# Kernel tuning notes

Hardware: AMD Instinct MI355X
Metric: run time of the kernel (lower is better)

Reference implementation:

```python
import jax, jax.numpy as jnp
import numpy as np

B, T, C = 64, 384, 256
NH, NKV = 4, 2
HD = C // NH            # 64
NREP = NH // NKV        # 2
NE, TOPK = 8, 2
HID = int(8 / 3 * C)    # 682
EPS_RMS = 1e-6


def _rope_tables(t_len):
    inv_freq = 1.0 / (10000.0 ** (np.arange(0, HD, 2, dtype=np.float32) / HD))
    t = np.arange(t_len, dtype=np.float32)
    freqs = np.outer(t, inv_freq)                      # [T, HD/2]
    emb = np.concatenate([freqs, freqs], axis=-1)      # [T, HD]
    return jnp.asarray(np.cos(emb)), jnp.asarray(np.sin(emb))


def _rotate_half(x):
    h = x.shape[-1] // 2
    return jnp.concatenate([-x[..., h:], x[..., :h]], axis=-1)


def _rmsnorm(v, w):
    return v * jax.lax.rsqrt(jnp.mean(v * v, axis=-1, keepdims=True) + EPS_RMS) * w


def setup_inputs() -> dict:
    key = jax.random.key(0)
    ks = jax.random.split(key, 10)
    s = lambda k, shape: (jax.random.normal(k, shape, jnp.float32) * 0.02)
    return {
        "x": jax.random.normal(ks[0], (B, T, C), jnp.float32),
        "ln1_w": jnp.ones((C,), jnp.float32),
        "ln2_w": jnp.ones((C,), jnp.float32),
        "wq": s(ks[1], (NH * HD, C)),
        "wk": s(ks[2], (NKV * HD, C)),
        "wv": s(ks[3], (NKV * HD, C)),
        "wo": s(ks[4], (C, C)),
        "router_w": s(ks[5], (NE, C)),
        "w1": s(ks[6], (NE, HID, C)),
        "w2": s(ks[7], (NE, C, HID)),
        "w3": s(ks[8], (NE, HID, C)),
    }


def reference(x, ln1_w, ln2_w, wq, wk, wv, wo, router_w, w1, w2, w3):
    Bx, Tx, Cx = x.shape
    # --- attention sub-block ---
    h = _rmsnorm(x, ln1_w)
    q = (h @ wq.T).reshape(Bx, Tx, NH, HD).transpose(0, 2, 1, 3)    # [B,H,T,D]
    k = (h @ wk.T).reshape(Bx, Tx, NKV, HD).transpose(0, 2, 1, 3)   # [B,KV,T,D]
    v = (h @ wv.T).reshape(Bx, Tx, NKV, HD).transpose(0, 2, 1, 3)
    cos, sin = _rope_tables(Tx)
    cos, sin = cos[None, None], sin[None, None]
    q = q * cos + _rotate_half(q) * sin
    k = k * cos + _rotate_half(k) * sin
    k = jnp.repeat(k, NREP, axis=1)   # GQA: expand kv heads
    v = jnp.repeat(v, NREP, axis=1)
    scores = jnp.einsum('bhtd,bhsd->bhts', q, k) / jnp.sqrt(jnp.float32(HD))
    causal = jnp.tril(jnp.ones((Tx, Tx), dtype=bool))
    scores = jnp.where(causal[None, None], scores, jnp.float32(-1e30))
    att = jax.nn.softmax(scores, axis=-1)
    y = jnp.einsum('bhts,bhsd->bhtd', att, v).transpose(0, 2, 1, 3).reshape(Bx, Tx, Cx)
    x = x + y @ wo.T

    # --- MoE sub-block ---
    flat = _rmsnorm(x, ln2_w).reshape(-1, Cx)                  # [N, C]
    probs = jax.nn.softmax(flat @ router_w.T, axis=-1)         # [N, NE]
    tp, ti = jax.lax.top_k(probs, TOPK)
    tp = tp / (jnp.sum(tp, axis=-1, keepdims=True) + 1e-9)
    # per-token per-expert combine weight (0 if not selected)
    weights = jnp.sum(tp[..., None] * jax.nn.one_hot(ti, NE, dtype=flat.dtype), axis=1)  # [N, NE]
    out = jnp.zeros_like(flat)
    for e in range(NE):  # small fixed expert count
        hh = jax.nn.silu(flat @ w1[e].T) * (flat @ w3[e].T)
        out = out + weights[:, e:e + 1] * (hh @ w2[e].T)
    return x + out.reshape(Bx, Tx, Cx)
```

## Files before the change

kernel.cpp:

```cpp
#include <hip/hip_runtime.h>
#include <hip/hip_bf16.h>
#include <math.h>

typedef unsigned short u16t;
typedef __bf16 bf16x8 __attribute__((ext_vector_type(8)));
typedef float f32x4 __attribute__((ext_vector_type(4)));

#define NBATCH 64
#define NT 384
#define NC 256
#define NHID 682
#define NHIDP 704
#define NTOK (NBATCH * NT)
#define NSLOT (2 * NTOK + 1024)

#define SB0 196
#define SB1 (SB0 + 512)
#define SB2 (SB1 + 256)
#define SB3 (SB2 + 5632)
#define SB4 (SB3 + 5632)
#define SB5 (SB4 + 48)
#define SB6 (SB5 + NTOK / 4)

static __device__ __forceinline__ float bf2f(u16t u) { return __uint_as_float(((unsigned int)u) << 16); }
static __device__ __forceinline__ u16t f2bf(float f) { return __builtin_bit_cast(u16t, __float2bfloat16(f)); }

static __device__ __forceinline__ void gload16(const void* gp, void* lp) {
  __builtin_amdgcn_global_load_lds((const __attribute__((address_space(1))) void*)gp,
                                   (__attribute__((address_space(3))) void*)lp, 16, 0, 0);
}

static __device__ __forceinline__ void pipe_barrier_full() {
  asm volatile("s_waitcnt vmcnt(0) lgkmcnt(0)" ::: "memory");
  __builtin_amdgcn_s_barrier();
  asm volatile("" ::: "memory");
}


__global__ __launch_bounds__(256) void k_setup(const float* __restrict__ wq, const float* __restrict__ wk,
                                               const float* __restrict__ wv, const float* __restrict__ wo,
                                               const float* __restrict__ w1, const float* __restrict__ w2,
                                               const float* __restrict__ w3,
                                               const float* __restrict__ x, const float* __restrict__ ln1w,
                                               int* __restrict__ tok, float* __restrict__ tokw,
                                               int* __restrict__ ctrl,
                                               u16t* __restrict__ wqkvb, u16t* __restrict__ wob,
                                               u16t* __restrict__ w1p, u16t* __restrict__ w3p,
                                               u16t* __restrict__ w2p, float* __restrict__ rtab,
                                               u16t* __restrict__ h) {
  int blk = blockIdx.x, t = threadIdx.x;
  if (blk < SB0) {
    int i = blk * 256 + t;
    tok[i] = -1; tokw[i] = 0.f;
    if (blk == 0 && t < 64) ctrl[t] = 0;
  } else if (blk < SB1) {
    int i = (blk - SB0) * 256 + t;
    int row = i >> 8, col = i & 255;
    float s = (row < 256) ? wq[(size_t)row * 256 + col]
            : (row < 384) ? wk[(size_t)(row - 256) * 256 + col]
                          : wv[(size_t)(row - 384) * 256 + col];
    wqkvb[i] = f2bf(s);
  } else if (blk < SB2) {
    int i = (blk - SB1) * 256 + t;
    wob[i] = f2bf(wo[i]);
  } else if (blk < SB3) {
    int idx = (blk - SB2) * 256 + t;
    int kcol = idx & 255; int tmp = idx >> 8; int nrow = tmp % NHIDP; int e = tmp / NHIDP;
    if (nrow < NHID) {
      size_t src = ((size_t)e * NHID + nrow) * NC + kcol;
      w1p[idx] = f2bf(w1[src]); w3p[idx] = f2bf(w3[src]);
    } else { w1p[idx] = 0; w3p[idx] = 0; }
  } else if (blk < SB4) {
    int idx = (blk - SB3) * 256 + t;
    int kcol = idx % NHIDP; int tmp = idx / NHIDP; int nrow = tmp & 255; int e = tmp >> 8;
    w2p[idx] = (kcol < NHID) ? f2bf(w2[((size_t)e * NC + nrow) * NHID + kcol]) : (u16t)0;
  } else if (blk < SB5) {
    int i = (blk - SB4) * 256 + t;
    int tt = i >> 5, d = i & 31;
    float ang = (float)tt * powf(10000.f, -(float)d * (1.f / 32.f));
    float s, c; sincosf(ang, &s, &c);
    ((float2*)rtab)[i] = make_float2(c, s);
  } else {
    int w = t >> 6, l = t & 63;
    int n = (blk - SB5) * 4 + w;
    const float* xr = x + (size_t)n * NC;
    float4 xa = *(const float4*)(xr + l * 4);
    float ssq = xa.x * xa.x + xa.y * xa.y + xa.z * xa.z + xa.w * xa.w;
    for (int d = 1; d < 64; d <<= 1) ssq += __shfl_xor(ssq, d, 64);
    float rs = rsqrtf(ssq * (1.f / 256.f) + 1e-6f);
    float4 wa = *(const float4*)(ln1w + l * 4);
    ushort4 o;
    o.x = f2bf(xa.x * rs * wa.x);
    o.y = f2bf(xa.y * rs * wa.y);
    o.z = f2bf(xa.z * rs * wa.z);
    o.w = f2bf(xa.w * rs * wa.w);
    *(ushort4*)(h + (size_t)n * NC + l * 4) = o;
  }
}

__global__ __launch_bounds__(256) void k_rms_router(const float* __restrict__ xin,
                                                    const float* __restrict__ wg,
                                                    const float* __restrict__ rw,
                                                    u16t* __restrict__ flat,
                                                    int* __restrict__ eidx,
                                                    float* __restrict__ ew) {
  int w = threadIdx.x >> 6, l = threadIdx.x & 63;
  int n = blockIdx.x * 4 + w;
  const float* xr = xin + (size_t)n * NC;
  float4 xa = *(const float4*)(xr + l * 4);
  float ssq = xa.x * xa.x + xa.y * xa.y + xa.z * xa.z + xa.w * xa.w;
  for (int d = 1; d < 64; d <<= 1) ssq += __shfl_xor(ssq, d, 64);
  float rs = rsqrtf(ssq * (1.f / 256.f) + 1e-6f);
  float4 wa = *(const float4*)(wg + l * 4);
  float n0 = xa.x * rs * wa.x, n1 = xa.y * rs * wa.y;
  float n2 = xa.z * rs * wa.z, n3 = xa.w * rs * wa.w;
  ushort4 o; o.x = f2bf(n0); o.y = f2bf(n1); o.z = f2bf(n2); o.w = f2bf(n3);
  *(ushort4*)(flat + (size_t)n * NC + l * 4) = o;
  float acc[8];
  for (int e = 0; e < 8; e++) {
    float4 ra = *(const float4*)(rw + (size_t)e * NC + l * 4);
    acc[e] = n0 * ra.x + n1 * ra.y + n2 * ra.z + n3 * ra.w;
  }
  for (int e = 0; e < 8; e++)
    for (int d = 1; d < 64; d <<= 1) acc[e] += __shfl_xor(acc[e], d, 64);
  if (l == 0) {
    float mx = acc[0];
    for (int e = 1; e < 8; e++) mx = fmaxf(mx, acc[e]);
    float p[8], sum = 0.f;
    for (int e = 0; e < 8; e++) { p[e] = __expf(acc[e] - mx); sum += p[e]; }
    float inv = 1.f / sum;
    for (int e = 0; e < 8; e++) p[e] *= inv;
    int i0 = 0; float b0 = p[0];
    for (int e = 1; e < 8; e++) if (p[e] > b0) { b0 = p[e]; i0 = e; }
    int i1 = -1; float b1 = -1.f;
    for (int e = 0; e < 8; e++) if (e != i0 && p[e] > b1) { b1 = p[e]; i1 = e; }
    float s2 = 1.f / (b0 + b1 + 1e-9f);
    eidx[n * 2] = i0; eidx[n * 2 + 1] = i1;
    ew[n * 2] = b0 * s2; ew[n * 2 + 1] = b1 * s2;
  }
}

__global__ __launch_bounds__(256) void k_hist(const int* __restrict__ eidx, int* __restrict__ ctrl) {
  int* cnt = ctrl; int* offs = ctrl + 8; int* cursor = ctrl + 20; int* done = ctrl + 32;
  __shared__ int lh[8];
  if (threadIdx.x < 8) lh[threadIdx.x] = 0;
  __syncthreads();
  int base = blockIdx.x * 1024 + threadIdx.x;
  for (int i = 0; i < 4; i++) atomicAdd(&lh[eidx[base + i * 256]], 1);
  __syncthreads();
  if (threadIdx.x < 8) {
    atomicAdd(&cnt[threadIdx.x], lh[threadIdx.x]);
    __threadfence();
  }
  __syncthreads();
  if (threadIdx.x == 0) {
    int prev = atomicAdd(done, 1);
    if (prev == 47) {
      int off = 0;
      for (int e = 0; e < 8; e++) {
        int c_ = atomicAdd(&cnt[e], 0);
        offs[e] = off; cursor[e] = off;
        off += ((c_ + 127) >> 7) << 7;
      }
      offs[8] = off;
    }
  }
}

__global__ __launch_bounds__(256) void k_gemm_qkv(const u16t* __restrict__ A,
                                                  const u16t* __restrict__ Bw,
                                                  const float* __restrict__ rtab,
                                                  u16t* __restrict__ qkv) {
  __shared__ __align__(16) u16t sA[2][128 * 64];
  __shared__ __align__(16) u16t sB[2][128 * 64];
  int t = threadIdx.x;
  int m0 = blockIdx.y * 128, n0 = blockIdx.x * 128;
  int w = t >> 6, l = t & 63, quad = l >> 4, lq = l & 15;
  int wm = (w >> 1) * 64, wn = (w & 1) * 64;
  const u16t* aP[4]; const u16t* bP[4];
  for (int i = 0; i < 4; i++) {
    int c = i * 256 + t; int r = c >> 3; int g = (c & 7) ^ (r & 7);
    aP[i] = A + (size_t)(m0 + r) * NC + g * 8;
    bP[i] = Bw + (size_t)(n0 + r) * NC + g * 8;
  }
  auto stage = [&](int p, int k0) {
    for (int i = 0; i < 4; i++) {
      gload16(aP[i] + k0, sA[p] + (size_t)(i * 256 + t) * 8);
      gload16(bP[i] + k0, sB[p] + (size_t)(i * 256 + t) * 8);
    }
  };
  const f32x4 fz = {0.f, 0.f, 0.f, 0.f};
  f32x4 acc[4][4];
  for (int i = 0; i < 4; i++) for (int j = 0; j < 4; j++) acc[i][j] = fz;
  stage(0, 0);
  pipe_barrier_full();
  for (int kb = 0; kb < 4; kb++) {
    int p = kb & 1;
    if (kb < 3) stage(p ^ 1, (kb + 1) << 6);
    for (int kk = 0; kk < 2; kk++) {
      int gq = kk * 4 + quad;
      bf16x8 af[4], bf[4];
      for (int mi = 0; mi < 4; mi++) { int row = wm + mi * 16 + lq; af[mi] = *(const bf16x8*)(sA[p] + (row * 8 + (gq ^ (row & 7))) * 8); }
      for (int ni = 0; ni < 4; ni++) { int row = wn + ni * 16 + lq; bf[ni] = *(const bf16x8*)(sB[p] + (row * 8 + (gq ^ (row & 7))) * 8); }
      for (int mi = 0; mi < 4; mi++)
        for (int ni = 0; ni < 4; ni++)
          acc[mi][ni] = __builtin_amdgcn_mfma_f32_16x16x32_bf16(af[mi], bf[ni], acc[mi][ni], 0, 0, 0);
    }
    if (kb < 3) pipe_barrier_full();
  }
  int cb = (n0 + wn) >> 6;
  const float2* rt = (const float2*)rtab;
  for (int mi = 0; mi < 4; mi++)
    for (int r = 0; r < 4; r++) {
      int gm = m0 + wm + mi * 16 + quad * 4 + r;
      u16t* orow = qkv + (size_t)gm * 512 + n0 + wn;
      if (cb < 6) {
        int tt = gm % NT;
        for (int ni = 0; ni < 2; ni++) {
          int d = ni * 16 + lq;
          float2 cs = rt[tt * 32 + d];
          float x1 = acc[mi][ni][r], x2 = acc[mi][ni + 2][r];
          orow[d] = f2bf(x1 * cs.x - x2 * cs.y);
          orow[d + 32] = f2bf(x2 * cs.x + x1 * cs.y);
        }
      } else {
        for (int ni = 0; ni < 4; ni++) orow[ni * 16 + lq] = f2bf(acc[mi][ni][r]);
      }
    }
}

__global__ __launch_bounds__(256) void k_gemm_wo(const u16t* __restrict__ A,
                                                 const u16t* __restrict__ Bw,
                                                 const float* __restrict__ xin,
                                                 float* __restrict__ xo) {
  __shared__ __align__(16) u16t sA[2][128 * 64];
  __shared__ __align__(16) u16t sB[2][128 * 64];
  int t = threadIdx.x;
  int m0 = blockIdx.y * 128, n0 = blockIdx.x * 128;
  int w = t >> 6, l = t & 63, quad = l >> 4, lq = l & 15;
  int wm = (w >> 1) * 64, wn = (w & 1) * 64;
  const u16t* aP[4]; const u16t* bP[4];
  for (int i = 0; i < 4; i++) {
    int c = i * 256 + t; int r = c >> 3; int g = (c & 7) ^ (r & 7);
    aP[i] = A + (size_t)(m0 + r) * NC + g * 8;
    bP[i] = Bw + (size_t)(n0 + r) * NC + g * 8;
  }
  auto stage = [&](int p, int k0) {
    for (int i = 0; i < 4; i++) {
      gload16(aP[i] + k0, sA[p] + (size_t)(i * 256 + t) * 8);
      gload16(bP[i] + k0, sB[p] + (size_t)(i * 256 + t) * 8);
    }
  };
  const f32x4 fz = {0.f, 0.f, 0.f, 0.f};
  f32x4 acc[4][4];
  for (int i = 0; i < 4; i++) for (int j = 0; j < 4; j++) acc[i][j] = fz;
  stage(0, 0);
  pipe_barrier_full();
  for (int kb = 0; kb < 4; kb++) {
    int p = kb & 1;
    if (kb < 3) stage(p ^ 1, (kb + 1) << 6);
    for (int kk = 0; kk < 2; kk++) {
      int gq = kk * 4 + quad;
      bf16x8 af[4], bf[4];
      for (int mi = 0; mi < 4; mi++) { int row = wm + mi * 16 + lq; af[mi] = *(const bf16x8*)(sA[p] + (row * 8 + (gq ^ (row & 7))) * 8); }
      for (int ni = 0; ni < 4; ni++) { int row = wn + ni * 16 + lq; bf[ni] = *(const bf16x8*)(sB[p] + (row * 8 + (gq ^ (row & 7))) * 8); }
      for (int mi = 0; mi < 4; mi++)
        for (int ni = 0; ni < 4; ni++)
          acc[mi][ni] = __builtin_amdgcn_mfma_f32_16x16x32_bf16(af[mi], bf[ni], acc[mi][ni], 0, 0, 0);
    }
    if (kb < 3) pipe_barrier_full();
  }
  for (int mi = 0; mi < 4; mi++)
    for (int ni = 0; ni < 4; ni++) {
      int gn = n0 + wn + ni * 16 + lq;
      for (int r = 0; r < 4; r++) {
        int gm = m0 + wm + mi * 16 + quad * 4 + r;
        xo[(size_t)gm * NC + gn] = acc[mi][ni][r] + xin[(size_t)gm * NC + gn];
      }
    }
}

__global__ __launch_bounds__(256) void k_attn(const u16t* __restrict__ qkv,
                                              u16t* __restrict__ y) {
  __shared__ __align__(16) u16t sK[2][64 * 64];
  __shared__ __align__(16) u16t sVT[2][64 * 64];
  __shared__ __align__(16) u16t sP[4 * 32 * 64];
  int qt = blockIdx.x, h = blockIdx.y, b = blockIdx.z;
  int kvh = h >> 1;
  int t = threadIdx.x, w = t >> 6, l = t & 63, quad = l >> 4, lq = l & 15;
  int tb = qt * 128 + w * 32;
  bf16x8 qf[2][2];
  for (int mi = 0; mi < 2; mi++)
    for (int kk = 0; kk < 2; kk++)
      qf[mi][kk] = *(const bf16x8*)(qkv + ((size_t)(b * NT + tb + mi * 16 + lq)) * 512 + h * 64 + kk * 32 + quad * 8);
  const f32x4 fz = {0.f, 0.f, 0.f, 0.f};
  f32x4 accO[2][4];
  float mrow[2][4], lrow[2][4];
  for (int mi = 0; mi < 2; mi++)
    for (int ni = 0; ni < 4; ni++) accO[mi][ni] = fz;
  for (int mi = 0; mi < 2; mi++)
    for (int r = 0; r < 4; r++) { mrow[mi][r] = -1e30f; lrow[mi][r] = 0.f; }
  u16t* myP = sP + w * 2048;
  int nkt = (qt + 1) * 2;
  ushort4 vr0[2], vr1[2];
  auto stageK = [&](int p, int kt) {
    int s0 = kt * 64;
    for (int i = 0; i < 2; i++) {
      int c = i * 256 + t; int s = c >> 3; int g = (c & 7) ^ (s & 7);
      gload16(qkv + ((size_t)(b * NT + s0 + s)) * 512 + 256 + kvh * 64 + g * 8, sK[p] + (size_t)c * 8);
    }
  };
  auto vload = [&](int kt) {
    int s0 = kt * 64;
    for (int i = 0; i < 2; i++) {
      int pI = i * 256 + t; int s = pI & 63; int n0 = (pI >> 6) * 8;
      const u16t* vp = qkv + ((size_t)(b * NT + s0 + s)) * 512 + 384 + kvh * 64 + n0;
      vr0[i] = *(const ushort4*)vp; vr1[i] = *(const ushort4*)(vp + 4);
    }
  };
  auto vstore = [&](int p) {
    for (int i = 0; i < 2; i++) {
      int pI = i * 256 + t; int s = pI & 63; int n0 = (pI >> 6) * 8;
      u16t vv[8] = {vr0[i].x, vr0[i].y, vr0[i].z, vr0[i].w, vr1[i].x, vr1[i].y, vr1[i].z, vr1[i].w};
      for (int j = 0; j < 8; j++) {
        int nn = n0 + j;
        sVT[p][(nn * 8 + ((s >> 3) ^ (nn & 7))) * 8 + (s & 7)] = vv[j];
      }
    }
  };
  stageK(0, 0); vload(0); vstore(0);
  pipe_barrier_full();
  for (int kt = 0; kt < nkt; kt++) {
    int p = kt & 1;
    int s0 = kt * 64;
    bool more = (kt + 1 < nkt);
    if (more) { stageK(p ^ 1, kt + 1); vload(kt + 1); }
    if (s0 <= tb + 31) {
      f32x4 accS[2][4];
      for (int mi = 0; mi < 2; mi++) for (int ni = 0; ni < 4; ni++) accS[mi][ni] = fz;
      for (int kk = 0; kk < 2; kk++) {
        int gq = kk * 4 + quad;
        bf16x8 kf[4];
        for (int ni = 0; ni < 4; ni++) { int row = ni * 16 + lq; kf[ni] = *(const bf16x8*)(sK[p] + (row * 8 + (gq ^ (row & 7))) * 8); }
        for (int mi = 0; mi < 2; mi++)
          for (int ni = 0; ni < 4; ni++)
            accS[mi][ni] = __builtin_amdgcn_mfma_f32_16x16x32_bf16(qf[mi][kk], kf[ni], accS[mi][ni], 0, 0, 0);
      }
      for (int mi = 0; mi < 2; mi++) {
        float alpha[4];
        for (int r = 0; r < 4; r++) {
          int trow = tb + mi * 16 + quad * 4 + r;
          float mx = -1e30f;
          for (int ni = 0; ni < 4; ni++) {
            int ss = s0 + ni * 16 + lq;
            float sv = accS[mi][ni][r] * 0.125f;
            sv = (ss > trow) ? -1e30f : sv;
            accS[mi][ni][r] = sv;
            mx = fmaxf(mx, sv);
          }
          for (int d = 1; d < 16; d <<= 1) mx = fmaxf(mx, __shfl_xor(mx, d, 64));
          float mnew = fmaxf(mrow[mi][r], mx);
          float al = __expf(mrow[mi][r] - mnew);
          float rsum = 0.f;
          for (int ni = 0; ni < 4; ni++) {
            float p2 = __expf(accS[mi][ni][r] - mnew);
            accS[mi][ni][r] = p2;
            rsum += p2;
          }
          for (int d = 1; d < 16; d <<= 1) rsum += __shfl_xor(rsum, d, 64);
          lrow[mi][r] = lrow[mi][r] * al + rsum;
          mrow[mi][r] = mnew;
          alpha[r] = al;
        }
        for (int ni = 0; ni < 4; ni++)
          for (int r = 0; r < 4; r++) accO[mi][ni][r] *= alpha[r];
        for (int ni = 0; ni < 4; ni++) {
          int cc = ni * 16 + lq;
          for (int r = 0; r < 4; r++) {
            int row = mi * 16 + quad * 4 + r;
            myP[((cc >> 3) * 32 + row) * 8 + (cc & 7)] = f2bf(accS[mi][ni][r]);
          }
        }
      }
      asm volatile("s_waitcnt lgkmcnt(0)" ::: "memory");
      for (int kk = 0; kk < 2; kk++) {
        int gq = kk * 4 + quad;
        bf16x8 pf[2], vf[4];
        for (int mi = 0; mi < 2; mi++) { int row = mi * 16 + lq; pf[mi] = *(const bf16x8*)(myP + (gq * 32 + row) * 8); }
        for (int ni = 0; ni < 4; ni++) { int row = ni * 16 + lq; vf[ni] = *(const bf16x8*)(sVT[p] + (row * 8 + (gq ^ (row & 7))) * 8); }
        for (int mi = 0; mi < 2; mi++)
          for (int ni = 0; ni < 4; ni++)
            accO[mi][ni] = __builtin_amdgcn_mfma_f32_16x16x32_bf16(pf[mi], vf[ni], accO[mi][ni], 0, 0, 0);
      }
    }
    if (more) {
      vstore(p ^ 1);
      pipe_barrier_full();
    }
  }
  for (int mi = 0; mi < 2; mi++)
    for (int r = 0; r < 4; r++) {
      int trow = tb + mi * 16 + quad * 4 + r;
      float inv = 1.f / lrow[mi][r];
      for (int ni = 0; ni < 4; ni++) {
        int d = ni * 16 + lq;
        y[((size_t)(b * NT + trow)) * NC + h * 64 + d] = f2bf(accO[mi][ni][r] * inv);
      }
    }
}

__global__ __launch_bounds__(256) void k_scatter(const int* __restrict__ eidx, const float* __restrict__ ew,
                                                 int* __restrict__ cursor, int* __restrict__ tok,
                                                 float* __restrict__ tokw, int* __restrict__ t2s) {
  __shared__ int lcnt[8], lbase[8];
  if (threadIdx.x < 8) lcnt[threadIdx.x] = 0;
  __syncthreads();
  int n = blockIdx.x * 256 + threadIdx.x;
  int e0 = eidx[n * 2], e1 = eidx[n * 2 + 1];
  int p0 = atomicAdd(&lcnt[e0], 1);
  int p1 = atomicAdd(&lcnt[e1], 1);
  __syncthreads();
  if (threadIdx.x < 8) lbase[threadIdx.x] = atomicAdd(&cursor[threadIdx.x], lcnt[threadIdx.x]);
  __syncthreads();
  int g0 = lbase[e0] + p0, g1 = lbase[e1] + p1;
  tok[g0] = n; tokw[g0] = ew[n * 2];
  tok[g1] = n; tokw[g1] = ew[n * 2 + 1];
  t2s[n * 2] = g0; t2s[n * 2 + 1] = g1;
}

__global__ __launch_bounds__(256) void k_moe_e1(const u16t* __restrict__ flat,
                                                const u16t* __restrict__ w1p,
                                                const u16t* __restrict__ w3p,
                                                const int* __restrict__ offs,
                                                const int* __restrict__ tok,
                                                u16t* __restrict__ hh) {
  __shared__ __align__(16) u16t sA[128 * 64];
  __shared__ __align__(16) u16t sB1[64 * 64];
  __shared__ __align__(16) u16t sB3[64 * 64];
  int t = threadIdx.x;
  int bid = blockIdx.x;
  int work = (bid & 7) * 539 + (bid >> 3);
  int sb = work / 11;
  int slot0 = sb * 128, n0 = (work - sb * 11) * 64;
  int e = 7;
  for (int i = 0; i < 8; i++) { if (slot0 < offs[i + 1]) { e = i; break; } }
  const u16t* B1 = w1p + (size_t)e * NHIDP * NC;
  const u16t* B3 = w3p + (size_t)e * NHIDP * NC;
  int w = t >> 6, l = t & 63, quad = l >> 4, lq = l & 15;
  int wm = (w >> 1) * 64, wn = (w & 1) * 32;
  const u16t* aP[4]; const u16t* b1P[2]; const u16t* b3P[2];
  for (int i = 0; i < 4; i++) {
    int c = i * 256 + t; int r = c >> 3; int g = (c & 7) ^ (r & 7);
    int tk = tok[slot0 + r]; int row = (tk < 0) ? 0 : tk;
    aP[i] = flat + (size_t)row * NC + g * 8;
  }
  for (int i = 0; i < 2; i++) {
    int c = i * 256 + t; int r = c >> 3; int g = (c & 7) ^ (r & 7);
    b1P[i] = B1 + (size_t)(n0 + r) * NC + g * 8;
    b3P[i] = B3 + (size_t)(n0 + r) * NC + g * 8;
  }
  const f32x4 fz = {0.f, 0.f, 0.f, 0.f};
  f32x4 a1[4][2], a3[4][2];
  for (int i = 0; i < 4; i++) for (int j = 0; j < 2; j++) { a1[i][j] = fz; a3[i][j] = fz; }
  for (int kb = 0; kb < 4; kb++) {
    int k0 = kb << 6;
    for (int i = 0; i < 4; i++)
      gload16(aP[i] + k0, sA + (size_t)(i * 256 + t) * 8);
    for (int i = 0; i < 2; i++) {
      gload16(b1P[i] + k0, sB1 + (size_t)(i * 256 + t) * 8);
      gload16(b3P[i] + k0, sB3 + (size_t)(i * 256 + t) * 8);
    }
    __syncthreads();
    for (int kk = 0; kk < 2; kk++) {
      int gq = kk * 4 + quad;
      bf16x8 af[4], b1f[2], b3f[2];
      for (int mi = 0; mi < 4; mi++) { int row = wm + mi * 16 + lq; af[mi] = *(const bf16x8*)(sA + (row * 8 + (gq ^ (row & 7))) * 8); }
      for (int ni = 0; ni < 2; ni++) {
        int row = wn + ni * 16 + lq;
        b1f[ni] = *(const bf16x8*)(sB1 + (row * 8 + (gq ^ (row & 7))) * 8);
        b3f[ni] = *(const bf16x8*)(sB3 + (row * 8 + (gq ^ (row & 7))) * 8);
      }
      for (int mi = 0; mi < 4; mi++)
        for (int ni = 0; ni < 2; ni++) {
          a1[mi][ni] = __builtin_amdgcn_mfma_f32_16x16x32_bf16(af[mi], b1f[ni], a1[mi][ni], 0, 0, 0);
          a3[mi][ni] = __builtin_amdgcn_mfma_f32_16x16x32_bf16(af[mi], b3f[ni], a3[mi][ni], 0, 0, 0);
        }
    }
    __syncthreads();
  }
  for (int mi = 0; mi < 4; mi++)
    for (int ni = 0; ni < 2; ni++) {
      int gn = n0 + wn + ni * 16 + lq;
      for (int r = 0; r < 4; r++) {
        int slot = slot0 + wm + mi * 16 + quad * 4 + r;
        float v1 = a1[mi][ni][r], v3 = a3[mi][ni][r];
        float hv = v1 / (1.f + __expf(-v1)) * v3;
        hh[(size_t)slot * NHIDP + gn] = f2bf(hv);
      }
    }
}

__global__ __launch_bounds__(256) void k_moe_e2(const u16t* __restrict__ hh,
                                                const u16t* __restrict__ w2p,
                                                const int* __restrict__ offs,
                                                const float* __restrict__ tokw,
                                                u16t* __restrict__ eo) {
  __shared__ __align__(16) u16t sA[2][128 * 64];
  __shared__ __align__(16) u16t sB[2][128 * 64];
  int t = threadIdx.x;
  int bid = blockIdx.x;
  int work = (bid & 7) * 98 + (bid >> 3);
  int slot0 = (work >> 1) * 128, n0 = (work & 1) * 128;
  int e = 7;
  for (int i = 0; i < 8; i++) { if (slot0 < offs[i + 1]) { e = i; break; } }
  const u16t* Bw = w2p + (size_t)e * NC * NHIDP;
  int w = t >> 6, l = t & 63, quad = l >> 4, lq = l & 15;
  int wm = (w >> 1) * 64, wn = (w & 1) * 64;
  const u16t* aP[4]; const u16t* bP[4];
  for (int i = 0; i < 4; i++) {
    int c = i * 256 + t; int r = c >> 3; int g = (c & 7) ^ (r & 7);
    aP[i] = hh + (size_t)(slot0 + r) * NHIDP + g * 8;
    bP[i] = Bw + (size_t)(n0 + r) * NHIDP + g * 8;
  }
  auto stage = [&](int p, int k0) {
    for (int i = 0; i < 4; i++) {
      gload16(aP[i] + k0, sA[p] + (size_t)(i * 256 + t) * 8);
      gload16(bP[i] + k0, sB[p] + (size_t)(i * 256 + t) * 8);
    }
  };
  const f32x4 fz = {0.f, 0.f, 0.f, 0.f};
  f32x4 acc[4][4];
  for (int i = 0; i < 4; i++) for (int j = 0; j < 4; j++) acc[i][j] = fz;
  stage(0, 0);
  pipe_barrier_full();
  for (int kb = 0; kb < 11; kb++) {
    int p = kb & 1;
    if (kb < 10) stage(p ^ 1, (kb + 1) << 6);
    for (int kk = 0; kk < 2; kk++) {
      int gq = kk * 4 + quad;
      bf16x8 af[4], bf[4];
      for (int mi = 0; mi < 4; mi++) { int row = wm + mi * 16 + lq; af[mi] = *(const bf16x8*)(sA[p] + (row * 8 + (gq ^ (row & 7))) * 8); }
      for (int ni = 0; ni < 4; ni++) { int row = wn + ni * 16 + lq; bf[ni] = *(const bf16x8*)(sB[p] + (row * 8 + (gq ^ (row & 7))) * 8); }
      for (int mi = 0; mi < 4; mi++)
        for (int ni = 0; ni < 4; ni++)
          acc[mi][ni] = __builtin_amdgcn_mfma_f32_16x16x32_bf16(af[mi], bf[ni], acc[mi][ni], 0, 0, 0);
    }
    if (kb < 10) pipe_barrier_full();
  }
  for (int mi = 0; mi < 4; mi++)
    for (int r = 0; r < 4; r++) {
      int slot = slot0 + wm + mi * 16 + quad * 4 + r;
      float wgt = tokw[slot];
      for (int ni = 0; ni < 4; ni++) {
        int gn = n0 + wn + ni * 16 + lq;
        eo[(size_t)slot * NC + gn] = f2bf(wgt * acc[mi][ni][r]);
      }
    }
}

__global__ __launch_bounds__(256) void k_combine(const u16t* __restrict__ eo,
                                                 const int* __restrict__ t2s,
                                                 float* __restrict__ xo) {
  int w = threadIdx.x >> 6, l = threadIdx.x & 63;
  int n = blockIdx.x * 4 + w;
  int g0 = t2s[n * 2], g1 = t2s[n * 2 + 1];
  float* xr = xo + (size_t)n * NC + l * 4;
  float4 xa = *(const float4*)xr;
  ushort4 a = *(const ushort4*)(eo + (size_t)g0 * NC + l * 4);
  ushort4 b = *(const ushort4*)(eo + (size_t)g1 * NC + l * 4);
  xa.x += bf2f(a.x) + bf2f(b.x);
  xa.y += bf2f(a.y) + bf2f(b.y);
  xa.z += bf2f(a.z) + bf2f(b.z);
  xa.w += bf2f(a.w) + bf2f(b.w);
  *(float4*)xr = xa;
}

extern "C" void kernel_launch(void* const* d_in, const int* in_sizes, int n_in,
                              void* d_out, int out_size, void* d_ws, size_t ws_size,
                              hipStream_t stream) {
  (void)in_sizes; (void)n_in; (void)out_size; (void)ws_size;
  const float* x    = (const float*)d_in[0];
  const float* ln1w = (const float*)d_in[1];
  const float* ln2w = (const float*)d_in[2];
  const float* wq   = (const float*)d_in[3];
  const float* wk   = (const float*)d_in[4];
  const float* wv   = (const float*)d_in[5];
  const float* wo   = (const float*)d_in[6];
  const float* rw   = (const float*)d_in[7];
  const float* w1   = (const float*)d_in[8];
  const float* w2   = (const float*)d_in[9];
  const float* w3   = (const float*)d_in[10];
  float* xo = (float*)d_out;

  char* ws = (char*)d_ws;
  size_t off = 0;
  int* ctrl  = (int*)(ws + off);  off += 4096;
  int* eidx  = (int*)(ws + off);  off += (size_t)NTOK * 2 * 4;
  float* ew  = (float*)(ws + off); off += (size_t)NTOK * 2 * 4;
  int* tok   = (int*)(ws + off);  off += (size_t)NSLOT * 4;
  float* tokw = (float*)(ws + off); off += (size_t)NSLOT * 4;
  int* t2s   = (int*)(ws + off);  off += (size_t)NTOK * 2 * 4;
  u16t* wqkvb = (u16t*)(ws + off); off += (size_t)512 * 256 * 2;
  u16t* wob  = (u16t*)(ws + off); off += (size_t)256 * 256 * 2;
  u16t* w1p  = (u16t*)(ws + off); off += (size_t)8 * NHIDP * NC * 2;
  u16t* w3p  = (u16t*)(ws + off); off += (size_t)8 * NHIDP * NC * 2;
  u16t* w2p  = (u16t*)(ws + off); off += (size_t)8 * NC * NHIDP * 2;
  float* rtab = (float*)(ws + off); off += (size_t)NT * 32 * 2 * 4;
  u16t* h    = (u16t*)(ws + off); off += (size_t)NTOK * NC * 2;
  u16t* qkv  = (u16t*)(ws + off); off += (size_t)NTOK * 512 * 2;
  u16t* y    = (u16t*)(ws + off); off += (size_t)NTOK * NC * 2;
  u16t* flat = (u16t*)(ws + off); off += (size_t)NTOK * NC * 2;
  u16t* hh   = (u16t*)(ws + off); off += (size_t)NSLOT * NHIDP * 2;
  u16t* eo   = h;
  int* offs = ctrl + 8; int* cursor = ctrl + 20;

  k_setup<<<SB6, 256, 0, stream>>>(wq, wk, wv, wo, w1, w2, w3, x, ln1w,
                                   tok, tokw, ctrl, wqkvb, wob, w1p, w3p, w2p, rtab, h);
  k_gemm_qkv<<<dim3(4, NTOK / 128), 256, 0, stream>>>(h, wqkvb, rtab, qkv);
  k_attn<<<dim3(3, 4, NBATCH), 256, 0, stream>>>(qkv, y);
  k_gemm_wo<<<dim3(2, NTOK / 128), 256, 0, stream>>>(y, wob, x, xo);

  k_rms_router<<<NTOK / 4, 256, 0, stream>>>(xo, ln2w, rw, flat, eidx, ew);
  k_hist<<<48, 256, 0, stream>>>(eidx, ctrl);
  k_scatter<<<NTOK / 256, 256, 0, stream>>>(eidx, ew, cursor, tok, tokw, t2s);
  k_moe_e1<<<4312, 256, 0, stream>>>(flat, w1p, w3p, offs, tok, hh);
  k_moe_e2<<<784, 256, 0, stream>>>(hh, w2p, offs, tokw, eo);
  k_combine<<<NTOK / 4, 256, 0, stream>>>(eo, t2s, xo);
}
```

Measured before the change: 292.0 us.

## Double-buffer LDS tiles in MoE expert up-projection kernel with K=32 stages

Restructures the w1/w3 grouped GEMM main loop to use two LDS buffers with 32-wide K tiles, issuing the global-to-LDS loads for the next stage before computing on the current one. The swizzle changes from 8 to 4 groups per row to match the narrower tile. The aim is to hide global load latency behind MFMA work and drop one of the two barriers per iteration. In exchange the loop runs twice as many iterations with less compute per barrier, so synchronisation overhead may rise.

```diff
diff --git a/kernel.cpp b/kernel.cpp
--- a/kernel.cpp
+++ b/kernel.cpp
@@ -434,9 +434,9 @@
                                                 const int* __restrict__ offs,
                                                 const int* __restrict__ tok,
                                                 u16t* __restrict__ hh) {
-  __shared__ __align__(16) u16t sA[128 * 64];
-  __shared__ __align__(16) u16t sB1[64 * 64];
-  __shared__ __align__(16) u16t sB3[64 * 64];
+  __shared__ __align__(16) u16t sA[2][128 * 32];
+  __shared__ __align__(16) u16t sB1[2][64 * 32];
+  __shared__ __align__(16) u16t sB3[2][64 * 32];
   int t = threadIdx.x;
   int bid = blockIdx.x;
   int work = (bid & 7) * 539 + (bid >> 3);
@@ -448,45 +448,47 @@
   const u16t* B3 = w3p + (size_t)e * NHIDP * NC;
   int w = t >> 6, l = t & 63, quad = l >> 4, lq = l & 15;
   int wm = (w >> 1) * 64, wn = (w & 1) * 32;
-  const u16t* aP[4]; const u16t* b1P[2]; const u16t* b3P[2];
-  for (int i = 0; i < 4; i++) {
-    int c = i * 256 + t; int r = c >> 3; int g = (c & 7) ^ (r & 7);
+  const u16t* aP[2]; const u16t* b1P; const u16t* b3P;
+  for (int i = 0; i < 2; i++) {
+    int c = i * 256 + t; int r = c >> 2; int g = (c & 3) ^ ((r >> 1) & 3);
     int tk = tok[slot0 + r]; int row = (tk < 0) ? 0 : tk;
     aP[i] = flat + (size_t)row * NC + g * 8;
   }
-  for (int i = 0; i < 2; i++) {
-    int c = i * 256 + t; int r = c >> 3; int g = (c & 7) ^ (r & 7);
-    b1P[i] = B1 + (size_t)(n0 + r) * NC + g * 8;
-    b3P[i] = B3 + (size_t)(n0 + r) * NC + g * 8;
-  }
+  {
+    int r = t >> 2; int g = (t & 3) ^ ((r >> 1) & 3);
+    b1P = B1 + (size_t)(n0 + r) * NC + g * 8;
+    b3P = B3 + (size_t)(n0 + r) * NC + g * 8;
+  }
+  auto stage = [&](int p, int k0) {
+    for (int i = 0; i < 2; i++)
+      gload16(aP[i] + k0, sA[p] + (size_t)(i * 256 + t) * 8);
+    gload16(b1P + k0, sB1[p] + (size_t)t * 8);
+    gload16(b3P + k0, sB3[p] + (size_t)t * 8);
+  };
   const f32x4 fz = {0.f, 0.f, 0.f, 0.f};
   f32x4 a1[4][2], a3[4][2];
   for (int i = 0; i < 4; i++) for (int j = 0; j < 2; j++) { a1[i][j] = fz; a3[i][j] = fz; }
-  for (int kb = 0; kb < 4; kb++) {
-    int k0 = kb << 6;
-    for (int i = 0; i < 4; i++)
-      gload16(aP[i] + k0, sA + (size_t)(i * 256 + t) * 8);
-    for (int i = 0; i < 2; i++) {
-      gload16(b1P[i] + k0, sB1 + (size_t)(i * 256 + t) * 8);
-      gload16(b3P[i] + k0, sB3 + (size_t)(i * 256 + t) * 8);
-    }
-    __syncthreads();
-    for (int kk = 0; kk < 2; kk++) {
-      int gq = kk * 4 + quad;
-      bf16x8 af[4], b1f[2], b3f[2];
-      for (int mi = 0; mi < 4; mi++) { int row = wm + mi * 16 + lq; af[mi] = *(const bf16x8*)(sA + (row * 8 + (gq ^ (row & 7))) * 8); }
+  stage(0, 0);
+  pipe_barrier_full();
+  for (int kb = 0; kb < 8; kb++) {
+    int p = kb & 1;
+    if (kb < 7) stage(p ^ 1, (kb + 1) << 5);
+    bf16x8 af[4], b1f[2], b3f[2];
+    for (int mi = 0; mi < 4; mi++) {
+      int row = wm + mi * 16 + lq;
+      af[mi] = *(const bf16x8*)(sA[p] + (row * 4 + (quad ^ ((row >> 1) & 3))) * 8);
+    }
+    for (int ni = 0; ni < 2; ni++) {
+      int row = wn + ni * 16 + lq;
+      b1f[ni] = *(const bf16x8*)(sB1[p] + (row * 4 + (quad ^ ((row >> 1) & 3))) * 8);
+      b3f[ni] = *(const bf16x8*)(sB3[p] + (row * 4 + (quad ^ ((row >> 1) & 3))) * 8);
+    }
+    for (int mi = 0; mi < 4; mi++)
       for (int ni = 0; ni < 2; ni++) {
-        int row = wn + ni * 16 + lq;
-        b1f[ni] = *(const bf16x8*)(sB1 + (row * 8 + (gq ^ (row & 7))) * 8);
-        b3f[ni] = *(const bf16x8*)(sB3 + (row * 8 + (gq ^ (row & 7))) * 8);
-      }
-      for (int mi = 0; mi < 4; mi++)
-        for (int ni = 0; ni < 2; ni++) {
-          a1[mi][ni] = __builtin_amdgcn_mfma_f32_16x16x32_bf16(af[mi], b1f[ni], a1[mi][ni], 0, 0, 0);
-          a3[mi][ni] = __builtin_amdgcn_mfma_f32_16x16x32_bf16(af[mi], b3f[ni], a3[mi][ni], 0, 0, 0);
-        }
-    }
-    __syncthreads();
+        a1[mi][ni] = __builtin_amdgcn_mfma_f32_16x16x32_bf16(af[mi], b1f[ni], a1[mi][ni], 0, 0, 0);
+        a3[mi][ni] = __builtin_amdgcn_mfma_f32_16x16x32_bf16(af[mi], b3f[ni], a3[mi][ni], 0, 0, 0);
+      }
+    if (kb < 7) pipe_barrier_full();
   }
   for (int mi = 0; mi < 4; mi++)
     for (int ni = 0; ni < 2; ni++) {
```

After: 305.1 us. +4.5%, slower.
